# Kernel tuning notes

Hardware: AMD Instinct MI355X
Metric: run time of the kernel (lower is better)

The kernel has to match this reference:

```python
import jax, jax.numpy as jnp
import numpy as np

K = 20  # neighbors

def _graph_feature(x, k):
    # x: (B, N, 3) -> (B, 3, N, k) neighbor features (DGCNN-style gather)
    inner = -2.0 * jnp.einsum('bnd,bmd->bnm', x, x)
    xx = jnp.sum(x * x, axis=2, keepdims=True)              # (B, N, 1)
    pairwise = -xx - inner - jnp.swapaxes(xx, 1, 2)          # (B, N, N) = -||xi-xj||^2
    _, idx = jax.lax.top_k(pairwise, k)                      # (B, N, k) nearest neighbors
    feat = jax.vmap(lambda xb, ib: xb[ib])(x, idx)           # (B, N, k, 3)
    return jnp.transpose(feat, (0, 3, 1, 2))                 # (B, 3, N, k)

def _vn_layer(x, w, scale, shift):
    # matmul over channel dim, folded-BN affine, relu
    y = jnp.einsum('oc,bcnk->bonk', w, x)
    y = y * scale[None, :, None, None] + shift[None, :, None, None]
    return jax.nn.relu(y)

def setup_inputs() -> dict:
    key = jax.random.key(0)
    ks = jax.random.split(key, 12)
    B, N = 32, 256
    inp = {
        'x': jax.random.normal(ks[0], (B, N, 3), dtype=jnp.float32),
        'w1': jax.random.normal(ks[1], (64, 3), dtype=jnp.float32),
        's1': jnp.ones((64,), jnp.float32), 't1': jnp.zeros((64,), jnp.float32),
        'w2': jax.random.normal(ks[2], (128, 64), dtype=jnp.float32) * 0.1,
        's2': jnp.ones((128,), jnp.float32), 't2': jnp.zeros((128,), jnp.float32),
        'w3': jax.random.normal(ks[3], (256, 128), dtype=jnp.float32) * 0.1,
        's3': jnp.ones((256,), jnp.float32), 't3': jnp.zeros((256,), jnp.float32),
        'fc1_w': jax.random.normal(ks[4], (128, 256), dtype=jnp.float32) * 0.05,
        'fc1_b': jnp.zeros((128,), jnp.float32),
        'fc2_w': jax.random.normal(ks[5], (40, 128), dtype=jnp.float32) * 0.05,
        'fc2_b': jnp.zeros((40,), jnp.float32),
    }
    return inp

def reference(x, w1, s1, t1, w2, s2, t2, w3, s3, t3, fc1_w, fc1_b, fc2_w, fc2_b):
    h = _graph_feature(x, K)                                 # (B, 3, N, k)
    h = jax.nn.relu(_vn_layer(h, w1, s1, t1))                # double relu as in source
    h = jax.nn.relu(_vn_layer(h, w2, s2, t2))
    h = jax.nn.relu(_vn_layer(h, w3, s3, t3))                # (B, 256, N, k)
    h = jnp.max(h, axis=-1)                                  # (B, 256, N) with N==256
    h = jax.nn.relu(h @ fc1_w.T + fc1_b)                     # Linear over last axis
    return h @ fc2_w.T + fc2_b                               # (B, 256, 40)
```

## Files before the change

kernel.cpp:

```cpp
#include <hip/hip_runtime.h>
#include <hip/hip_bf16.h>

#define B_ 32
#define N_ 256
#define K_ 20
#define C1 64
#define C2 128
#define C3 256
#define F1 128
#define F2 40
#define NEG_INF (-3.402823466e38f)

#define DPP_QUAD_XOR1 0xB1
#define DPP_QUAD_XOR2 0x4E
#define DPP_HALF_MIRR 0x141
#define DPP_ROW_MIRR  0x140
#define DPP_BCAST15   0x142
#define DPP_BCAST31   0x143

__device__ __forceinline__ unsigned wave_max_to_l63(unsigned v) {
    unsigned m;
    m = (unsigned)__builtin_amdgcn_update_dpp(0, (int)v, DPP_QUAD_XOR1, 0xF, 0xF, true);
    v = m > v ? m : v;
    m = (unsigned)__builtin_amdgcn_update_dpp(0, (int)v, DPP_QUAD_XOR2, 0xF, 0xF, true);
    v = m > v ? m : v;
    m = (unsigned)__builtin_amdgcn_update_dpp(0, (int)v, DPP_HALF_MIRR, 0xF, 0xF, true);
    v = m > v ? m : v;
    m = (unsigned)__builtin_amdgcn_update_dpp(0, (int)v, DPP_ROW_MIRR, 0xF, 0xF, true);
    v = m > v ? m : v;
    m = (unsigned)__builtin_amdgcn_update_dpp(0, (int)v, DPP_BCAST15, 0xF, 0xF, true);
    v = m > v ? m : v;
    m = (unsigned)__builtin_amdgcn_update_dpp(0, (int)v, DPP_BCAST31, 0xF, 0xF, true);
    v = m > v ? m : v;
    return v;
}

__global__ __launch_bounds__(256) void k_front(const float* __restrict__ x,
    const float* __restrict__ w1, const float* __restrict__ s1, const float* __restrict__ b1,
    const float* __restrict__ w2, const float* __restrict__ s2, const float* __restrict__ b2,
    const float* __restrict__ w3, const float* __restrict__ s3, const float* __restrict__ b3,
    const float* __restrict__ fc1w,
    int* __restrict__ idx, float* __restrict__ P, float* __restrict__ fc1T) {

    __shared__ float smem[3136];
    const int blk  = blockIdx.x;
    const int t    = threadIdx.x;
    const int lane = t & 63;
    const int wv   = t >> 6;

    if (blk < 512) {
        float* xs = smem;
        float* y1 = smem + 64;
        float* y2 = smem + 1088;
        const int pbase = blk * 16;
        const int og = t >> 2;
        const int p0 = (t & 3) * 4;

        if (t < 48) xs[t] = x[(size_t)pbase * 3 + t];
        __syncthreads();

        {
            const int oc = lane;
            const float wa = w1[oc * 3 + 0], wb = w1[oc * 3 + 1], wc = w1[oc * 3 + 2];
            const float sc = s1[oc], sh = b1[oc];
            const int q0 = wv * 4;
            float4 v;
            #pragma unroll
            for (int p = 0; p < 4; ++p) {
                const int pp = q0 + p;
                float vv = wa * xs[pp * 3 + 0] + wb * xs[pp * 3 + 1] + wc * xs[pp * 3 + 2];
                (&v.x)[p] = fmaxf(vv * sc + sh, 0.0f);
            }
            *(float4*)&y1[oc * 16 + q0] = v;
        }
        __syncthreads();

        {
            const int oc0 = og * 2;
            float acc[2][4] = {};
            for (int k = 0; k < C1; k += 4) {
                float4 a[4];
                #pragma unroll
                for (int kk = 0; kk < 4; ++kk)
                    a[kk] = *(const float4*)&y1[(k + kk) * 16 + p0];
                const float4 wA = *(const float4*)(w2 + (size_t)oc0 * C1 + k);
                const float4 wB = *(const float4*)(w2 + (size_t)(oc0 + 1) * C1 + k);
                #pragma unroll
                for (int kk = 0; kk < 4; ++kk) {
                    #pragma unroll
                    for (int p = 0; p < 4; ++p) {
                        acc[0][p] += (&wA.x)[kk] * (&a[kk].x)[p];
                        acc[1][p] += (&wB.x)[kk] * (&a[kk].x)[p];
                    }
                }
            }
            const float sc0 = s2[oc0], sh0 = b2[oc0];
            const float sc1 = s2[oc0 + 1], sh1 = b2[oc0 + 1];
            float4 v0, v1;
            #pragma unroll
            for (int p = 0; p < 4; ++p) {
                (&v0.x)[p] = fmaxf(acc[0][p] * sc0 + sh0, 0.0f);
                (&v1.x)[p] = fmaxf(acc[1][p] * sc1 + sh1, 0.0f);
            }
            *(float4*)&y2[oc0 * 16 + p0]       = v0;
            *(float4*)&y2[(oc0 + 1) * 16 + p0] = v1;
        }
        __syncthreads();

        {
            const int oc0 = og * 4;
            float acc[4][4] = {};
            for (int k = 0; k < C2; k += 4) {
                float4 a[4];
                #pragma unroll
                for (int kk = 0; kk < 4; ++kk)
                    a[kk] = *(const float4*)&y2[(k + kk) * 16 + p0];
                float4 w[4];
                #pragma unroll
                for (int o = 0; o < 4; ++o)
                    w[o] = *(const float4*)(w3 + (size_t)(oc0 + o) * C2 + k);
                #pragma unroll
                for (int o = 0; o < 4; ++o) {
                    #pragma unroll
                    for (int kk = 0; kk < 4; ++kk) {
                        const float wvv = (&w[o].x)[kk];
                        #pragma unroll
                        for (int p = 0; p < 4; ++p)
                            acc[o][p] += wvv * (&a[kk].x)[p];
                    }
                }
            }
            const float4 sc = *(const float4*)&s3[oc0];
            const float4 sh = *(const float4*)&b3[oc0];
            #pragma unroll
            for (int p = 0; p < 4; ++p) {
                float4 v;
                #pragma unroll
                for (int o = 0; o < 4; ++o)
                    (&v.x)[o] = fmaxf(acc[o][p] * (&sc.x)[o] + (&sh.x)[o], 0.0f);
                *(float4*)&P[(size_t)(pbase + p0 + p) * C3 + oc0] = v;
            }
        }

    } else if (blk < 2560) {
        const int tb = blk - 512;
        const int b  = tb >> 6;
        const int n  = ((tb & 63) << 2) | wv;
        const int bn = (b << 8) | n;
        const float* xb = x + (size_t)b * N_ * 3;

        const float nx = xb[n * 3 + 0], ny = xb[n * 3 + 1], nz = xb[n * 3 + 2];
        const float xxn = nx * nx + ny * ny + nz * nz;

        unsigned k0, k1, k2, k3;
        {
            unsigned kk[4];
            #pragma unroll
            for (int i = 0; i < 4; ++i) {
                const int m = lane + (i << 6);
                const float cx = xb[m * 3 + 0], cy = xb[m * 3 + 1], cz = xb[m * 3 + 2];
                const float xxm = cx * cx + cy * cy + cz * cz;
                const float v = 2.0f * (nx * cx + ny * cy + nz * cz) - xxn - xxm;
                const unsigned u = __float_as_uint(v);
                kk[i] = (u & 0x80000000u) ? ~u : (u | 0x80000000u);
            }
            k0 = kk[0]; k1 = kk[1]; k2 = kk[2]; k3 = kk[3];
        }

        int mine = (lane == 0) ? n : 0;
        if (lane == (n & 63)) {
            const int slot = n >> 6;
            if      (slot == 0) k0 = 0u;
            else if (slot == 1) k1 = 0u;
            else if (slot == 2) k2 = 0u;
            else                k3 = 0u;
        }

        #pragma unroll 1
        for (int it = 1; it < K_; ++it) {
            unsigned ra = k0 > k1 ? k0 : k1;
            unsigned rb = k2 > k3 ? k2 : k3;
            const unsigned full = wave_max_to_l63(ra > rb ? ra : rb);
            const unsigned M = (unsigned)__builtin_amdgcn_readlane((int)full, 63);
            const unsigned long long b0 = __ballot(k0 == M);
            const unsigned long long b1 = __ballot(k1 == M);
            const unsigned long long b2m = __ballot(k2 == M);
            const unsigned long long b3m = __ballot(k3 == M);
            int ri;
            if      (b0)  ri = __ffsll((long long)b0) - 1;
            else if (b1)  ri = 64  + __ffsll((long long)b1) - 1;
            else if (b2m) ri = 128 + __ffsll((long long)b2m) - 1;
            else          ri = 192 + __ffsll((long long)b3m) - 1;
            if (lane == it) mine = ri;
            if (lane == (ri & 63)) {
                const int slot = ri >> 6;
                if      (slot == 0) k0 = 0u;
                else if (slot == 1) k1 = 0u;
                else if (slot == 2) k2 = 0u;
                else                k3 = 0u;
            }
        }
        if (lane < K_) idx[(size_t)bn * K_ + lane] = mine;

    } else {
        const int g = (blk - 2560) * 256 + t;
        #pragma unroll
        for (int i = 0; i < 8; ++i) {
            const int e = g + i * 4096;
            const int j = e >> 8, n = e & 255;
            fc1T[n * F1 + j] = fc1w[e];
        }
    }
}

__global__ __launch_bounds__(256) void k_gfc(const float* __restrict__ P,
                                             const int* __restrict__ idx,
                                             const float* __restrict__ fc1T,
                                             const float* __restrict__ fc1b,
                                             const float* __restrict__ fc2w,
                                             const float* __restrict__ fc2b,
                                             float* __restrict__ out) {
    const int b    = blockIdx.x >> 4;
    const int ch0  = (blockIdx.x & 15) * 16;
    const int t    = threadIdx.x;
    const int lane = t & 63;

    __shared__ float Ht[N_ * 16];
    __shared__ float gl[16 * 132];
    __shared__ float w2l[F2 * 129];

    for (int e = t; e < F2 * F1; e += 256)
        w2l[(e >> 7) * 129 + (e & 127)] = fc2w[e];

    {
        const int q  = t & 3;
        const int nl = t >> 2;
        const float* Pq = P + (size_t)b * N_ * C3 + ch0 + q * 4;
        #pragma unroll
        for (int r = 0; r < 4; ++r) {
            const int n = r * 64 + nl;
            const int* ib = idx + ((size_t)((b << 8) | n)) * K_;
            float4 m = make_float4(NEG_INF, NEG_INF, NEG_INF, NEG_INF);
            #pragma unroll
            for (int j = 0; j < K_; ++j) {
                const int id = ib[j];
                const float4 p = *(const float4*)(Pq + (size_t)id * C3);
                m.x = fmaxf(m.x, p.x);
                m.y = fmaxf(m.y, p.y);
                m.z = fmaxf(m.z, p.z);
                m.w = fmaxf(m.w, p.w);
            }
            *(float4*)&Ht[n * 16 + q * 4] = m;
        }
    }
    __syncthreads();

    {
        const int c0 = (t >> 6) * 4;
        float acc[2][4] = {};
        #pragma unroll 4
        for (int n = 0; n < N_; ++n) {
            const float2 w = *(const float2*)&fc1T[n * F1 + lane * 2];
            const float4 a = *(const float4*)&Ht[n * 16 + c0];
            #pragma unroll
            for (int c = 0; c < 4; ++c) {
                acc[0][c] += w.x * (&a.x)[c];
                acc[1][c] += w.y * (&a.x)[c];
            }
        }
        const float bb0 = fc1b[lane * 2], bb1 = fc1b[lane * 2 + 1];
        #pragma unroll
        for (int c = 0; c < 4; ++c) {
            float2 v;
            v.x = fmaxf(acc[0][c] + bb0, 0.0f);
            v.y = fmaxf(acc[1][c] + bb1, 0.0f);
            *(float2*)&gl[(c0 + c) * 132 + lane * 2] = v;
        }
    }
    __syncthreads();

    for (int o = t; o < 16 * F2; o += 256) {
        const int ci = o / F2;
        const int m  = o % F2;
        float acc = fc2b[m];
        const float* wr = w2l + m * 129;
        const float* gr = gl + ci * 132;
        #pragma unroll 4
        for (int j = 0; j < F1; ++j)
            acc += wr[j] * gr[j];
        out[((size_t)(b * C3 + ch0 + ci)) * F2 + m] = acc;
    }
}

extern "C" void kernel_launch(void* const* d_in, const int* in_sizes, int n_in,
                              void* d_out, int out_size, void* d_ws, size_t ws_size,
                              hipStream_t stream) {
    const float* x    = (const float*)d_in[0];
    const float* w1   = (const float*)d_in[1];
    const float* s1   = (const float*)d_in[2];
    const float* t1   = (const float*)d_in[3];
    const float* w2   = (const float*)d_in[4];
    const float* s2   = (const float*)d_in[5];
    const float* t2   = (const float*)d_in[6];
    const float* w3   = (const float*)d_in[7];
    const float* s3   = (const float*)d_in[8];
    const float* t3   = (const float*)d_in[9];
    const float* fc1w = (const float*)d_in[10];
    const float* fc1b = (const float*)d_in[11];
    const float* fc2w = (const float*)d_in[12];
    const float* fc2b = (const float*)d_in[13];
    float* out = (float*)d_out;

    char* ws = (char*)d_ws;
    int*   idx  = (int*)ws;
    float* P    = (float*)(ws + (size_t)B_ * N_ * K_ * 4);
    float* fc1T = P + (size_t)B_ * N_ * C3;

    k_front<<<2576, 256, 0, stream>>>(x, w1, s1, t1, w2, s2, t2, w3, s3, t3,
                                      fc1w, idx, P, fc1T);
    k_gfc<<<B_ * 16, 256, 0, stream>>>(P, idx, fc1T, fc1b, fc2w, fc2b, out);
}
```

Baseline: 131.9 us.

## Replace iterative argmax top-k with radix threshold select and compact fc2

Result: no change. 129.4 us (-1.9%).

```diff
diff --git a/kernel.cpp b/kernel.cpp
--- a/kernel.cpp
+++ b/kernel.cpp
@@ -11,30 +11,6 @@
 #define F2 40
 #define NEG_INF (-3.402823466e38f)
 
-#define DPP_QUAD_XOR1 0xB1
-#define DPP_QUAD_XOR2 0x4E
-#define DPP_HALF_MIRR 0x141
-#define DPP_ROW_MIRR  0x140
-#define DPP_BCAST15   0x142
-#define DPP_BCAST31   0x143
-
-__device__ __forceinline__ unsigned wave_max_to_l63(unsigned v) {
-    unsigned m;
-    m = (unsigned)__builtin_amdgcn_update_dpp(0, (int)v, DPP_QUAD_XOR1, 0xF, 0xF, true);
-    v = m > v ? m : v;
-    m = (unsigned)__builtin_amdgcn_update_dpp(0, (int)v, DPP_QUAD_XOR2, 0xF, 0xF, true);
-    v = m > v ? m : v;
-    m = (unsigned)__builtin_amdgcn_update_dpp(0, (int)v, DPP_HALF_MIRR, 0xF, 0xF, true);
-    v = m > v ? m : v;
-    m = (unsigned)__builtin_amdgcn_update_dpp(0, (int)v, DPP_ROW_MIRR, 0xF, 0xF, true);
-    v = m > v ? m : v;
-    m = (unsigned)__builtin_amdgcn_update_dpp(0, (int)v, DPP_BCAST15, 0xF, 0xF, true);
-    v = m > v ? m : v;
-    m = (unsigned)__builtin_amdgcn_update_dpp(0, (int)v, DPP_BCAST31, 0xF, 0xF, true);
-    v = m > v ? m : v;
-    return v;
-}
-
 __global__ __launch_bounds__(256) void k_front(const float* __restrict__ x,
     const float* __restrict__ w1, const float* __restrict__ s1, const float* __restrict__ b1,
     const float* __restrict__ w2, const float* __restrict__ s2, const float* __restrict__ b2,
@@ -167,52 +143,55 @@
             k0 = kk[0]; k1 = kk[1]; k2 = kk[2]; k3 = kk[3];
         }
 
-        int mine = (lane == 0) ? n : 0;
-        if (lane == (n & 63)) {
-            const int slot = n >> 6;
-            if      (slot == 0) k0 = 0u;
-            else if (slot == 1) k1 = 0u;
-            else if (slot == 2) k2 = 0u;
-            else                k3 = 0u;
-        }
-
-        #pragma unroll 1
-        for (int it = 1; it < K_; ++it) {
-            unsigned ra = k0 > k1 ? k0 : k1;
-            unsigned rb = k2 > k3 ? k2 : k3;
-            const unsigned full = wave_max_to_l63(ra > rb ? ra : rb);
-            const unsigned M = (unsigned)__builtin_amdgcn_readlane((int)full, 63);
-            const unsigned long long b0 = __ballot(k0 == M);
-            const unsigned long long b1 = __ballot(k1 == M);
-            const unsigned long long b2m = __ballot(k2 == M);
-            const unsigned long long b3m = __ballot(k3 == M);
-            int ri;
-            if      (b0)  ri = __ffsll((long long)b0) - 1;
-            else if (b1)  ri = 64  + __ffsll((long long)b1) - 1;
-            else if (b2m) ri = 128 + __ffsll((long long)b2m) - 1;
-            else          ri = 192 + __ffsll((long long)b3m) - 1;
-            if (lane == it) mine = ri;
-            if (lane == (ri & 63)) {
-                const int slot = ri >> 6;
-                if      (slot == 0) k0 = 0u;
-                else if (slot == 1) k1 = 0u;
-                else if (slot == 2) k2 = 0u;
-                else                k3 = 0u;
-            }
-        }
-        if (lane < K_) idx[(size_t)bn * K_ + lane] = mine;
+        unsigned prefix = 0u;
+        #pragma unroll
+        for (int bit = 30; bit >= 0; --bit) {
+            const unsigned cand = prefix | (1u << bit);
+            const int c = __popcll(__ballot(k0 >= cand))
+                        + __popcll(__ballot(k1 >= cand))
+                        + __popcll(__ballot(k2 >= cand))
+                        + __popcll(__ballot(k3 >= cand));
+            if (c >= K_) prefix = cand;
+        }
+        const unsigned T = prefix;
+
+        int* op = idx + (size_t)bn * K_;
+        const unsigned long long lt = (1ull << lane) - 1ull;
+
+        const unsigned long long G0 = __ballot(k0 > T);
+        const unsigned long long G1 = __ballot(k1 > T);
+        const unsigned long long G2 = __ballot(k2 > T);
+        const unsigned long long G3 = __ballot(k3 > T);
+        const int n0 = __popcll(G0), n1 = __popcll(G1), n2 = __popcll(G2), n3 = __popcll(G3);
+        const int g = n0 + n1 + n2 + n3;
+        if (k0 > T) op[          __popcll(G0 & lt)] = lane;
+        if (k1 > T) op[n0      + __popcll(G1 & lt)] = 64  | lane;
+        if (k2 > T) op[n0 + n1 + __popcll(G2 & lt)] = 128 | lane;
+        if (k3 > T) op[n0 + n1 + n2 + __popcll(G3 & lt)] = 192 | lane;
+
+        const int e = K_ - g;
+        const unsigned long long E0 = __ballot(k0 == T);
+        const unsigned long long E1 = __ballot(k1 == T);
+        const unsigned long long E2 = __ballot(k2 == T);
+        const unsigned long long E3 = __ballot(k3 == T);
+        const int m0 = __popcll(E0), m1 = __popcll(E1), m2 = __popcll(E2);
+        if (k0 == T) { const int p = __popcll(E0 & lt);                 if (p < e) op[g + p] = lane; }
+        if (k1 == T) { const int p = m0 + __popcll(E1 & lt);            if (p < e) op[g + p] = 64  | lane; }
+        if (k2 == T) { const int p = m0 + m1 + __popcll(E2 & lt);       if (p < e) op[g + p] = 128 | lane; }
+        if (k3 == T) { const int p = m0 + m1 + m2 + __popcll(E3 & lt);  if (p < e) op[g + p] = 192 | lane; }
 
     } else {
         const int g = (blk - 2560) * 256 + t;
         #pragma unroll
         for (int i = 0; i < 8; ++i) {
             const int e = g + i * 4096;
-            const int j = e >> 8, n = e & 255;
-            fc1T[n * F1 + j] = fc1w[e];
+            const int j = e >> 8, nn = e & 255;
+            fc1T[nn * F1 + j] = fc1w[e];
         }
     }
 }
 
+#define GLT_S 20
 __global__ __launch_bounds__(256) void k_gfc(const float* __restrict__ P,
                                              const int* __restrict__ idx,
                                              const float* __restrict__ fc1T,
@@ -226,7 +205,7 @@
     const int lane = t & 63;
 
     __shared__ float Ht[N_ * 16];
-    __shared__ float gl[16 * 132];
+    __shared__ float glT[F1 * GLT_S];
     __shared__ float w2l[F2 * 129];
 
     for (int e = t; e < F2 * F1; e += 256)
@@ -269,26 +248,40 @@
             }
         }
         const float bb0 = fc1b[lane * 2], bb1 = fc1b[lane * 2 + 1];
+        float4 va, vb;
         #pragma unroll
         for (int c = 0; c < 4; ++c) {
-            float2 v;
-            v.x = fmaxf(acc[0][c] + bb0, 0.0f);
-            v.y = fmaxf(acc[1][c] + bb1, 0.0f);
-            *(float2*)&gl[(c0 + c) * 132 + lane * 2] = v;
-        }
+            (&va.x)[c] = fmaxf(acc[0][c] + bb0, 0.0f);
+            (&vb.x)[c] = fmaxf(acc[1][c] + bb1, 0.0f);
+        }
+        *(float4*)&glT[(lane * 2)     * GLT_S + c0] = va;
+        *(float4*)&glT[(lane * 2 + 1) * GLT_S + c0] = vb;
     }
     __syncthreads();
 
-    for (int o = t; o < 16 * F2; o += 256) {
-        const int ci = o / F2;
-        const int m  = o % F2;
-        float acc = fc2b[m];
-        const float* wr = w2l + m * 129;
-        const float* gr = gl + ci * 132;
-        #pragma unroll 4
-        for (int j = 0; j < F1; ++j)
-            acc += wr[j] * gr[j];
-        out[((size_t)(b * C3 + ch0 + ci)) * F2 + m] = acc;
+    {
+        const int m   = t & 63;
+        const int cig = t >> 6;
+        if (m < F2) {
+            float a0 = 0.f, a1 = 0.f, a2 = 0.f, a3 = 0.f;
+            const float* wr = w2l + m * 129;
+            const float* gp = glT + cig * 4;
+            #pragma unroll 4
+            for (int j = 0; j < F1; ++j) {
+                const float w = wr[j];
+                const float4 gv = *(const float4*)(gp + j * GLT_S);
+                a0 += w * gv.x;
+                a1 += w * gv.y;
+                a2 += w * gv.z;
+                a3 += w * gv.w;
+            }
+            const float bb = fc2b[m];
+            const size_t rb = (size_t)(b * C3 + ch0 + cig * 4) * F2 + m;
+            out[rb]          = a0 + bb;
+            out[rb + F2]     = a1 + bb;
+            out[rb + 2 * F2] = a2 + bb;
+            out[rb + 3 * F2] = a3 + bb;
+        }
     }
 }
 
```
